# Optimization experiments

Measured on AMD Instinct MI355X. Metric: run time of the kernel, lower is better.

Reference implementation:

```python
import jax, jax.numpy as jnp
import numpy as np

N_NODES = 50000
N_EDGES = 800000
IN_FEATS = 64
HIDDEN = 32
HEADS = 8
NEG_SLOPE = 0.2


def gat_conv(x, W, a_l, a_r, b, src, dst, num_nodes):
    """DGL-style GATConv. x:[N,in], W:[in,H,O], a_l/a_r/b:[H,O]. Returns [N,H,O]."""
    feat = jnp.einsum('ni,iho->nho', x, W)              # [N,H,O]
    el = jnp.sum(feat * a_l, axis=-1)                   # [N,H]
    er = jnp.sum(feat * a_r, axis=-1)                   # [N,H]
    e = jax.nn.leaky_relu(el[src] + er[dst], NEG_SLOPE) # [E,H]
    # segment softmax over incoming edges of each dst node
    m = jax.ops.segment_max(e, dst, num_segments=num_nodes)   # [N,H]
    ex = jnp.exp(e - m[dst])                                   # [E,H]
    s = jax.ops.segment_sum(ex, dst, num_segments=num_nodes)   # [N,H]
    alpha = ex / s[dst]                                        # [E,H]
    out = jax.ops.segment_sum(feat[src] * alpha[:, :, None], dst,
                              num_segments=num_nodes)          # [N,H,O]
    return out + b


def setup_inputs() -> dict:
    key = jax.random.key(0)
    ks = jax.random.split(key, 12)
    g1 = 1.0 / np.sqrt(IN_FEATS)
    g2 = 1.0 / np.sqrt(HIDDEN * HEADS)
    return {
        'features': jax.random.normal(ks[0], (N_NODES, IN_FEATS), jnp.float32),
        'src': jax.random.randint(ks[1], (N_EDGES,), 0, N_NODES, jnp.int32),
        'dst': jax.random.randint(ks[2], (N_EDGES,), 0, N_NODES, jnp.int32),
        'edge_types': jax.random.randint(ks[3], (N_EDGES,), 0, 4, jnp.int32),
        'W1': jax.random.normal(ks[4], (IN_FEATS, HEADS, HIDDEN), jnp.float32) * g1,
        'al1': jax.random.normal(ks[5], (HEADS, HIDDEN), jnp.float32) * g1,
        'ar1': jax.random.normal(ks[6], (HEADS, HIDDEN), jnp.float32) * g1,
        'b1': jnp.zeros((HEADS, HIDDEN), jnp.float32),
        'W2': jax.random.normal(ks[7], (HIDDEN * HEADS, 1, 1), jnp.float32) * g2,
        'al2': jax.random.normal(ks[8], (1, 1), jnp.float32) * g2,
        'ar2': jax.random.normal(ks[9], (1, 1), jnp.float32) * g2,
        'b2': jnp.zeros((1, 1), jnp.float32),
    }


def reference(features, src, dst, edge_types, W1, al1, ar1, b1, W2, al2, ar2, b2):
    h = gat_conv(features, W1, al1, ar1, b1, src, dst, N_NODES)  # [N,H,O]
    h = jax.nn.relu(h.reshape(h.shape[0], -1))                   # [N,H*O]
    h = gat_conv(h, W2, al2, ar2, b2, src, dst, N_NODES)         # [N,1,1]
    h = jnp.squeeze(h, axis=1)                                   # [N,1]
    return jax.nn.sigmoid(h)
```

## Files before the change

### kernel.cpp

```cpp
#include <hip/hip_runtime.h>

#define N_NODES 50000
#define N_EDGES 800000
#define FEAT_BLOCKS 3125
#define SCAT_BLOCKS 1563
#define CAP 64

typedef unsigned int uint32;
typedef unsigned short ushort16;
typedef unsigned char uchar8;
typedef short bf8v __attribute__((ext_vector_type(8)));
typedef float f32x4 __attribute__((ext_vector_type(4)));

__device__ __forceinline__ ushort16 f2bf(float f) {
  uint32 u = __float_as_uint(f);
  u += 0x7fffu + ((u >> 16) & 1u);
  return (ushort16)(u >> 16);
}

__global__ __launch_bounds__(256) void k_init(const float* __restrict__ W1,
    ushort16* __restrict__ w1t, int4* __restrict__ deg4) {
  int b = blockIdx.x, t = threadIdx.x;
  if (b < 64) {
    int col = b * 4 + (t >> 6), k = t & 63;
    w1t[col * 64 + k] = f2bf(W1[k * 256 + col]);
  } else {
    int i = (b - 64) * 256 + t;
    if (i < 12500) deg4[i] = make_int4(0, 0, 0, 0);
  }
}

__global__ __launch_bounds__(256) void k_build_feat(const float* __restrict__ x,
    const ushort16* __restrict__ w1t, const float* __restrict__ al1,
    const float* __restrict__ ar1, uchar8* __restrict__ feat8,
    float* __restrict__ el1, float* __restrict__ er1,
    const int* __restrict__ src, const int* __restrict__ dst,
    int* __restrict__ deg, unsigned short* __restrict__ esrc16) {
  int t = threadIdx.x;
  int r3 = blockIdx.x % 3;
  if (r3 == 2) {
    int e0 = (blockIdx.x / 3) * 512 + t;
    int e1 = e0 + 256;
    if (e0 < N_EDGES) {
      int d0 = dst[e0];
      int s0 = src[e0];
      int p0 = atomicAdd(&deg[d0], 1);
      if (p0 < CAP) esrc16[d0 * CAP + p0] = (unsigned short)s0;
    }
    if (e1 < N_EDGES) {
      int d1 = dst[e1];
      int s1 = src[e1];
      int p1 = atomicAdd(&deg[d1], 1);
      if (p1 < CAP) esrc16[d1 * CAP + p1] = (unsigned short)s1;
    }
    return;
  }
  int fidx = (blockIdx.x / 3) * 2 + r3;
  if (fidx >= FEAT_BLOCKS) return;
  int w = t >> 6, lane = t & 63;
  int quad = lane >> 4, m = lane & 15;
  int n0 = fidx * 16;
  const float* xr = x + (n0 + m) * 64 + quad * 8;
  float4 xa = *(const float4*)(xr);
  float4 xbv = *(const float4*)(xr + 4);
  float4 xc = *(const float4*)(xr + 32);
  float4 xd = *(const float4*)(xr + 36);
  bf8v a0, a1;
  a0[0] = (short)f2bf(xa.x); a0[1] = (short)f2bf(xa.y);
  a0[2] = (short)f2bf(xa.z); a0[3] = (short)f2bf(xa.w);
  a0[4] = (short)f2bf(xbv.x); a0[5] = (short)f2bf(xbv.y);
  a0[6] = (short)f2bf(xbv.z); a0[7] = (short)f2bf(xbv.w);
  a1[0] = (short)f2bf(xc.x); a1[1] = (short)f2bf(xc.y);
  a1[2] = (short)f2bf(xc.z); a1[3] = (short)f2bf(xc.w);
  a1[4] = (short)f2bf(xd.x); a1[5] = (short)f2bf(xd.y);
  a1[6] = (short)f2bf(xd.z); a1[7] = (short)f2bf(xd.w);
  float pl0[4] = {0.f, 0.f, 0.f, 0.f}, pr0[4] = {0.f, 0.f, 0.f, 0.f};
  float pl1[4] = {0.f, 0.f, 0.f, 0.f}, pr1[4] = {0.f, 0.f, 0.f, 0.f};
#pragma unroll
  for (int nt = 0; nt < 4; ++nt) {
    int colg = w * 64 + nt * 16 + m;
    const bf8v* bw = (const bf8v*)(w1t + colg * 64 + quad * 8);
    bf8v b0 = bw[0];
    bf8v b1 = bw[4];
    f32x4 acc = {0.f, 0.f, 0.f, 0.f};
    acc = __builtin_amdgcn_mfma_f32_16x16x32_bf16(a0, b0, acc, 0, 0, 0);
    acc = __builtin_amdgcn_mfma_f32_16x16x32_bf16(a1, b1, acc, 0, 0, 0);
    float al = al1[colg], ar = ar1[colg];
#pragma unroll
    for (int i = 0; i < 4; ++i) {
      uint32 pb = (uint32)__builtin_amdgcn_cvt_pk_fp8_f32(acc[i], acc[i], 0, 0);
      feat8[(size_t)(n0 + quad * 4 + i) * 256 + colg] = (uchar8)(pb & 0xffu);
      if (nt < 2) { pl0[i] += acc[i] * al; pr0[i] += acc[i] * ar; }
      else        { pl1[i] += acc[i] * al; pr1[i] += acc[i] * ar; }
    }
  }
#pragma unroll
  for (int off = 1; off < 16; off <<= 1) {
#pragma unroll
    for (int i = 0; i < 4; ++i) {
      pl0[i] += __shfl_xor(pl0[i], off, 64);
      pr0[i] += __shfl_xor(pr0[i], off, 64);
      pl1[i] += __shfl_xor(pl1[i], off, 64);
      pr1[i] += __shfl_xor(pr1[i], off, 64);
    }
  }
  if (m == 0) {
#pragma unroll
    for (int i = 0; i < 4; ++i) {
      int n = n0 + quad * 4 + i;
      el1[n * 8 + 2 * w] = pl0[i];
      er1[n * 8 + 2 * w] = pr0[i];
      el1[n * 8 + 2 * w + 1] = pl1[i];
      er1[n * 8 + 2 * w + 1] = pr1[i];
    }
  }
}

#define ACC8F8(u, ex)                                                    \
  {                                                                      \
    auto p0 = __builtin_amdgcn_cvt_pk_f32_fp8((u).x, 0);                 \
    auto p1 = __builtin_amdgcn_cvt_pk_f32_fp8((u).x, 1);                 \
    auto p2 = __builtin_amdgcn_cvt_pk_f32_fp8((u).y, 0);                 \
    auto p3 = __builtin_amdgcn_cvt_pk_f32_fp8((u).y, 1);                 \
    acc[0] += p0[0] * (ex); acc[1] += p0[1] * (ex);                      \
    acc[2] += p1[0] * (ex); acc[3] += p1[1] * (ex);                      \
    acc[4] += p2[0] * (ex); acc[5] += p2[1] * (ex);                      \
    acc[6] += p3[0] * (ex); acc[7] += p3[1] * (ex);                      \
  }

__global__ __launch_bounds__(256) void k_agg1(const int* __restrict__ deg,
    const unsigned short* __restrict__ esrc16, const uint2* __restrict__ featv,
    const float* __restrict__ el1, const float* __restrict__ er1,
    const float* __restrict__ b1, const float* __restrict__ W2,
    float* __restrict__ feat2) {
  int t = threadIdx.x, nl = t >> 5, lt = t & 31;
  int n = blockIdx.x * 8 + nl;
  int h = lt >> 2;
  int begin = n * CAP;
  int d = deg[n]; d = d > CAP ? CAP : d;
  int end = begin + d;
  float er_h = er1[n * 8 + h];
  float acc[8] = {0.f, 0.f, 0.f, 0.f, 0.f, 0.f, 0.f, 0.f};
  float s = 0.f;
  int e = begin;
  for (; e + 8 <= end; e += 8) {
    uint4 sv = *(const uint4*)(esrc16 + e);
    int sn[8] = {(int)(sv.x & 0xffffu), (int)(sv.x >> 16),
                 (int)(sv.y & 0xffffu), (int)(sv.y >> 16),
                 (int)(sv.z & 0xffffu), (int)(sv.z >> 16),
                 (int)(sv.w & 0xffffu), (int)(sv.w >> 16)};
    uint2 u[8];
    float ex[8];
#pragma unroll
    for (int j = 0; j < 8; ++j) u[j] = featv[sn[j] * 32 + lt];
#pragma unroll
    for (int j = 0; j < 8; ++j) {
      float v = el1[sn[j] * 8 + h] + er_h;
      v = v > 0.f ? v : 0.2f * v;
      ex[j] = __expf(v);
      s += ex[j];
    }
#pragma unroll
    for (int j = 0; j < 8; ++j) ACC8F8(u[j], ex[j]);
  }
  for (; e + 4 <= end; e += 4) {
    int sn[4];
    uint2 u[4];
    float ex[4];
#pragma unroll
    for (int j = 0; j < 4; ++j) sn[j] = (int)esrc16[e + j];
#pragma unroll
    for (int j = 0; j < 4; ++j) u[j] = featv[sn[j] * 32 + lt];
#pragma unroll
    for (int j = 0; j < 4; ++j) {
      float v = el1[sn[j] * 8 + h] + er_h;
      v = v > 0.f ? v : 0.2f * v;
      ex[j] = __expf(v);
      s += ex[j];
    }
#pragma unroll
    for (int j = 0; j < 4; ++j) ACC8F8(u[j], ex[j]);
  }
  for (; e < end; ++e) {
    int s0 = (int)esrc16[e];
    uint2 u0 = featv[s0 * 32 + lt];
    float v0 = el1[s0 * 8 + h] + er_h;
    v0 = v0 > 0.f ? v0 : 0.2f * v0;
    float ex0 = __expf(v0);
    s += ex0;
    ACC8F8(u0, ex0);
  }
  float inv = (d > 0) ? 1.f / s : 0.f;
  int o = lt * 8;
  float4 bb0 = *(const float4*)(b1 + o), bb1 = *(const float4*)(b1 + o + 4);
  float4 ww0 = *(const float4*)(W2 + o), ww1 = *(const float4*)(W2 + o + 4);
  float r = fmaxf(acc[0] * inv + bb0.x, 0.f) * ww0.x
          + fmaxf(acc[1] * inv + bb0.y, 0.f) * ww0.y
          + fmaxf(acc[2] * inv + bb0.z, 0.f) * ww0.z
          + fmaxf(acc[3] * inv + bb0.w, 0.f) * ww0.w
          + fmaxf(acc[4] * inv + bb1.x, 0.f) * ww1.x
          + fmaxf(acc[5] * inv + bb1.y, 0.f) * ww1.y
          + fmaxf(acc[6] * inv + bb1.z, 0.f) * ww1.z
          + fmaxf(acc[7] * inv + bb1.w, 0.f) * ww1.w;
  __shared__ float red[256];
  red[t] = r;
  __syncthreads();
  for (int off = 16; off > 0; off >>= 1) {
    if (lt < off) red[t] += red[t + off];
    __syncthreads();
  }
  if (lt == 0) feat2[n] = red[t];
}

__global__ __launch_bounds__(256) void k_layer2(const int* __restrict__ deg,
    const unsigned short* __restrict__ esrc16, const float* __restrict__ feat2,
    const float* __restrict__ al2, const float* __restrict__ ar2,
    const float* __restrict__ b2, float* __restrict__ out) {
  int t = threadIdx.x, g = t >> 4, lt = t & 15;
  int n = blockIdx.x * 16 + g;
  int begin = n * CAP;
  int d = deg[n]; d = d > CAP ? CAP : d;
  int end = begin + d;
  float a2 = al2[0];
  float er_n = feat2[n] * ar2[0];
  float num = 0.f, s = 0.f;
  for (int e = begin + lt; e < end; e += 16) {
    int sN = (int)esrc16[e];
    float f = feat2[sN];
    float v = f * a2 + er_n;
    v = v > 0.f ? v : 0.2f * v;
    float ex = __expf(v);
    num += f * ex;
    s += ex;
  }
#pragma unroll
  for (int off = 8; off > 0; off >>= 1) {
    num += __shfl_down(num, off, 16);
    s += __shfl_down(s, off, 16);
  }
  if (lt == 0) {
    float val = (d > 0) ? num / s : 0.f;
    out[n] = 1.f / (1.f + __expf(-(val + b2[0])));
  }
}

extern "C" void kernel_launch(void* const* d_in, const int* in_sizes, int n_in,
                              void* d_out, int out_size, void* d_ws, size_t ws_size,
                              hipStream_t stream) {
  const float* x   = (const float*)d_in[0];
  const int* src   = (const int*)d_in[1];
  const int* dst   = (const int*)d_in[2];
  const float* W1  = (const float*)d_in[4];
  const float* al1 = (const float*)d_in[5];
  const float* ar1 = (const float*)d_in[6];
  const float* b1  = (const float*)d_in[7];
  const float* W2  = (const float*)d_in[8];
  const float* al2 = (const float*)d_in[9];
  const float* ar2 = (const float*)d_in[10];
  const float* b2  = (const float*)d_in[11];

  float* ws    = (float*)d_ws;
  float* el1   = ws;
  float* er1   = ws + 400000;
  float* feat2 = ws + 800000;
  int* deg     = (int*)ws + 850000;
  unsigned short* esrc16 = (unsigned short*)((int*)ws + 900000);
  ushort16* w1t  = (ushort16*)((int*)ws + 2500000);
  uchar8* feat8  = (uchar8*)((int*)ws + 2508192);

  k_init<<<64 + 49, 256, 0, stream>>>(W1, w1t, (int4*)deg);
  k_build_feat<<<FEAT_BLOCKS + SCAT_BLOCKS + 1, 256, 0, stream>>>(
      x, w1t, al1, ar1, feat8, el1, er1, src, dst, deg, esrc16);
  k_agg1<<<N_NODES / 8, 256, 0, stream>>>(deg, esrc16, (const uint2*)feat8,
                                          el1, er1, b1, W2, feat2);
  k_layer2<<<N_NODES / 16, 256, 0, stream>>>(deg, esrc16, feat2, al2, ar2, b2,
                                             (float*)d_out);
}
```

Before: 170.8 us.

## Drop init kernel: convert W1 inline, memset degrees, rebalance edge-scatter blocks

Removes the separate k_init kernel. W1 is now read in fp32 and converted to bf16 inside the feature GEMM, and the degree array is zeroed with hipMemsetAsync. The block interleave changes from 2 feature blocks per scatter block to 4, with each scatter block now handling 1024 edges instead of 512. This saves one kernel launch and a dependency step, but every feature block now does strided scalar global loads of W1 and the conversion, where before it did vectorized bf16 loads.

```diff
diff --git a/kernel.cpp b/kernel.cpp
--- a/kernel.cpp
+++ b/kernel.cpp
@@ -3,59 +3,42 @@
 #define N_NODES 50000
 #define N_EDGES 800000
 #define FEAT_BLOCKS 3125
-#define SCAT_BLOCKS 1563
 #define CAP 64
 
 typedef unsigned int uint32;
-typedef unsigned short ushort16;
 typedef unsigned char uchar8;
 typedef short bf8v __attribute__((ext_vector_type(8)));
 typedef float f32x4 __attribute__((ext_vector_type(4)));
 
-__device__ __forceinline__ ushort16 f2bf(float f) {
+__device__ __forceinline__ unsigned short f2bf(float f) {
   uint32 u = __float_as_uint(f);
   u += 0x7fffu + ((u >> 16) & 1u);
-  return (ushort16)(u >> 16);
-}
-
-__global__ __launch_bounds__(256) void k_init(const float* __restrict__ W1,
-    ushort16* __restrict__ w1t, int4* __restrict__ deg4) {
-  int b = blockIdx.x, t = threadIdx.x;
-  if (b < 64) {
-    int col = b * 4 + (t >> 6), k = t & 63;
-    w1t[col * 64 + k] = f2bf(W1[k * 256 + col]);
-  } else {
-    int i = (b - 64) * 256 + t;
-    if (i < 12500) deg4[i] = make_int4(0, 0, 0, 0);
-  }
+  return (unsigned short)(u >> 16);
 }
 
 __global__ __launch_bounds__(256) void k_build_feat(const float* __restrict__ x,
-    const ushort16* __restrict__ w1t, const float* __restrict__ al1,
+    const float* __restrict__ W1, const float* __restrict__ al1,
     const float* __restrict__ ar1, uchar8* __restrict__ feat8,
     float* __restrict__ el1, float* __restrict__ er1,
     const int* __restrict__ src, const int* __restrict__ dst,
     int* __restrict__ deg, unsigned short* __restrict__ esrc16) {
   int t = threadIdx.x;
-  int r3 = blockIdx.x % 3;
-  if (r3 == 2) {
-    int e0 = (blockIdx.x / 3) * 512 + t;
-    int e1 = e0 + 256;
-    if (e0 < N_EDGES) {
-      int d0 = dst[e0];
-      int s0 = src[e0];
-      int p0 = atomicAdd(&deg[d0], 1);
-      if (p0 < CAP) esrc16[d0 * CAP + p0] = (unsigned short)s0;
-    }
-    if (e1 < N_EDGES) {
-      int d1 = dst[e1];
-      int s1 = src[e1];
-      int p1 = atomicAdd(&deg[d1], 1);
-      if (p1 < CAP) esrc16[d1 * CAP + p1] = (unsigned short)s1;
+  int q = blockIdx.x / 5, r = blockIdx.x % 5;
+  if (r == 4) {
+    int e0 = q * 1024 + t;
+#pragma unroll
+    for (int j = 0; j < 4; ++j) {
+      int e = e0 + j * 256;
+      if (e < N_EDGES) {
+        int d = dst[e];
+        int sV = src[e];
+        int p = atomicAdd(&deg[d], 1);
+        if (p < CAP) esrc16[d * CAP + p] = (unsigned short)sV;
+      }
     }
     return;
   }
-  int fidx = (blockIdx.x / 3) * 2 + r3;
+  int fidx = q * 4 + r;
   if (fidx >= FEAT_BLOCKS) return;
   int w = t >> 6, lane = t & 63;
   int quad = lane >> 4, m = lane & 15;
@@ -79,9 +62,12 @@
 #pragma unroll
   for (int nt = 0; nt < 4; ++nt) {
     int colg = w * 64 + nt * 16 + m;
-    const bf8v* bw = (const bf8v*)(w1t + colg * 64 + quad * 8);
-    bf8v b0 = bw[0];
-    bf8v b1 = bw[4];
+    bf8v b0, b1;
+#pragma unroll
+    for (int j = 0; j < 8; ++j) {
+      b0[j] = (short)f2bf(W1[(quad * 8 + j) * 256 + colg]);
+      b1[j] = (short)f2bf(W1[(quad * 8 + j + 32) * 256 + colg]);
+    }
     f32x4 acc = {0.f, 0.f, 0.f, 0.f};
     acc = __builtin_amdgcn_mfma_f32_16x16x32_bf16(a0, b0, acc, 0, 0, 0);
     acc = __builtin_amdgcn_mfma_f32_16x16x32_bf16(a1, b1, acc, 0, 0, 0);
@@ -265,12 +251,12 @@
   float* feat2 = ws + 800000;
   int* deg     = (int*)ws + 850000;
   unsigned short* esrc16 = (unsigned short*)((int*)ws + 900000);
-  ushort16* w1t  = (ushort16*)((int*)ws + 2500000);
-  uchar8* feat8  = (uchar8*)((int*)ws + 2508192);
-
-  k_init<<<64 + 49, 256, 0, stream>>>(W1, w1t, (int4*)deg);
-  k_build_feat<<<FEAT_BLOCKS + SCAT_BLOCKS + 1, 256, 0, stream>>>(
-      x, w1t, al1, ar1, feat8, el1, er1, src, dst, deg, esrc16);
+  uchar8* feat8  = (uchar8*)((int*)ws + 2500000);
+
+  hipMemsetAsync(deg, 0, 50000 * sizeof(int), stream);
+
+  k_build_feat<<<3910, 256, 0, stream>>>(x, W1, al1, ar1, feat8, el1, er1,
+                                         src, dst, deg, esrc16);
   k_agg1<<<N_NODES / 8, 256, 0, stream>>>(deg, esrc16, (const uint2*)feat8,
                                           el1, er1, b1, W2, feat2);
   k_layer2<<<N_NODES / 16, 256, 0, stream>>>(deg, esrc16, feat2, al2, ar2, b2,
```

Result: no change. 171.7 us (+0.5%).

## Partition edge scatter by destination range across blocks to localize atomics

Applied to the files above, without the earlier changes.

Replaces the one-edge-per-thread scatter with blocks that each read an 8192-edge chunk using vectorized int4 loads and handle only edges whose destination falls in one of 8 node ranges. This is meant to keep the atomic counters and adjacency writes of each block in a compact region for better cache locality, and to interleave scatter blocks with feature blocks in a 32:8 ratio. In exchange, every edge is read 8 times, which adds global read traffic and branch work.

```diff
diff --git a/kernel.cpp b/kernel.cpp
--- a/kernel.cpp
+++ b/kernel.cpp
@@ -3,8 +3,9 @@
 #define N_NODES 50000
 #define N_EDGES 800000
 #define FEAT_BLOCKS 3125
-#define SCAT_BLOCKS 1563
 #define CAP 64
+#define NCHUNK 98
+#define RANGE 6250
 
 typedef unsigned int uint32;
 typedef unsigned short ushort16;
@@ -35,27 +36,36 @@
     const float* __restrict__ ar1, uchar8* __restrict__ feat8,
     float* __restrict__ el1, float* __restrict__ er1,
     const int* __restrict__ src, const int* __restrict__ dst,
-    int* __restrict__ deg, unsigned short* __restrict__ esrc16) {
+    int* __restrict__ deg, ushort16* __restrict__ esrc16) {
   int t = threadIdx.x;
-  int r3 = blockIdx.x % 3;
-  if (r3 == 2) {
-    int e0 = (blockIdx.x / 3) * 512 + t;
-    int e1 = e0 + 256;
-    if (e0 < N_EDGES) {
-      int d0 = dst[e0];
-      int s0 = src[e0];
-      int p0 = atomicAdd(&deg[d0], 1);
-      if (p0 < CAP) esrc16[d0 * CAP + p0] = (unsigned short)s0;
-    }
-    if (e1 < N_EDGES) {
-      int d1 = dst[e1];
-      int s1 = src[e1];
-      int p1 = atomicAdd(&deg[d1], 1);
-      if (p1 < CAP) esrc16[d1 * CAP + p1] = (unsigned short)s1;
+  int q = blockIdx.x / 40, r = blockIdx.x % 40;
+  if (r >= 32) {
+    int g = r - 32;
+    int lo = g * RANGE, hi = lo + RANGE;
+    int base = q * 8192;
+    const int4* dst4 = (const int4*)(dst + base);
+    const int4* src4 = (const int4*)(src + base);
+#pragma unroll
+    for (int it = 0; it < 8; ++it) {
+      int i4 = it * 256 + t;
+      int ebase = base + i4 * 4;
+      if (ebase >= N_EDGES) break;
+      int4 dv = dst4[i4];
+      int4 sv = src4[i4];
+      int dd[4] = {dv.x, dv.y, dv.z, dv.w};
+      int ss[4] = {sv.x, sv.y, sv.z, sv.w};
+#pragma unroll
+      for (int k = 0; k < 4; ++k) {
+        int d = dd[k];
+        if (d >= lo && d < hi) {
+          int p = atomicAdd(&deg[d], 1);
+          if (p < CAP) esrc16[d * CAP + p] = (ushort16)ss[k];
+        }
+      }
     }
     return;
   }
-  int fidx = (blockIdx.x / 3) * 2 + r3;
+  int fidx = q * 32 + r;
   if (fidx >= FEAT_BLOCKS) return;
   int w = t >> 6, lane = t & 63;
   int quad = lane >> 4, m = lane & 15;
@@ -129,7 +139,7 @@
   }
 
 __global__ __launch_bounds__(256) void k_agg1(const int* __restrict__ deg,
-    const unsigned short* __restrict__ esrc16, const uint2* __restrict__ featv,
+    const ushort16* __restrict__ esrc16, const uint2* __restrict__ featv,
     const float* __restrict__ el1, const float* __restrict__ er1,
     const float* __restrict__ b1, const float* __restrict__ W2,
     float* __restrict__ feat2) {
@@ -213,7 +223,7 @@
 }
 
 __global__ __launch_bounds__(256) void k_layer2(const int* __restrict__ deg,
-    const unsigned short* __restrict__ esrc16, const float* __restrict__ feat2,
+    const ushort16* __restrict__ esrc16, const float* __restrict__ feat2,
     const float* __restrict__ al2, const float* __restrict__ ar2,
     const float* __restrict__ b2, float* __restrict__ out) {
   int t = threadIdx.x, g = t >> 4, lt = t & 15;
@@ -264,13 +274,13 @@
   float* er1   = ws + 400000;
   float* feat2 = ws + 800000;
   int* deg     = (int*)ws + 850000;
-  unsigned short* esrc16 = (unsigned short*)((int*)ws + 900000);
+  ushort16* esrc16 = (ushort16*)((int*)ws + 900000);
   ushort16* w1t  = (ushort16*)((int*)ws + 2500000);
   uchar8* feat8  = (uchar8*)((int*)ws + 2508192);
 
   k_init<<<64 + 49, 256, 0, stream>>>(W1, w1t, (int4*)deg);
-  k_build_feat<<<FEAT_BLOCKS + SCAT_BLOCKS + 1, 256, 0, stream>>>(
-      x, w1t, al1, ar1, feat8, el1, er1, src, dst, deg, esrc16);
+  k_build_feat<<<3920, 256, 0, stream>>>(x, w1t, al1, ar1, feat8, el1, er1,
+                                         src, dst, deg, esrc16);
   k_agg1<<<N_NODES / 8, 256, 0, stream>>>(deg, esrc16, (const uint2*)feat8,
                                           el1, er1, b1, W2, feat2);
   k_layer2<<<N_NODES / 16, 256, 0, stream>>>(deg, esrc16, feat2, al2, ar2, b2,
```

Measured after the change: 181.1 us. +6.0%, slower.
